# Performance work log

Measured on AMD Instinct MI355X. Metric: run time of the kernel, lower is better.

Reference implementation:

```python
import jax, jax.numpy as jnp
import numpy as np

B, IN_DIM, HID, ATT = 16384, 128, 512, 256
TOTAL = IN_DIM + HID + ATT


def setup_inputs() -> dict:
    key = jax.random.key(0)
    ks = jax.random.split(key, 10)
    u = lambda k, shape, lo, hi: jax.random.uniform(k, shape, jnp.float32, lo, hi)
    return {
        "t": jnp.float32(0.0),
        "h_ltc": jax.random.normal(ks[0], (B, HID), jnp.float32),
        "x_t": jax.random.normal(ks[1], (B, IN_DIM), jnp.float32),
        "context": jax.random.normal(ks[2], (B, ATT), jnp.float32),
        "W_gd": u(ks[3], (2 * HID, TOTAL), -0.1, 0.1),
        "b_gd": u(ks[4], (2 * HID,), -0.1, 0.1),
        "W_tau": u(ks[5], (HID, HID), -0.1, 0.1),
        "b_tau": u(ks[6], (HID,), -0.1, 0.1),
        "gleak": u(ks[7], (HID,), 0.001, 1.0),
        "cm": u(ks[8], (HID,), 0.4, 0.6),
    }


def reference(t, h_ltc, x_t, context, W_gd, b_gd, W_tau, b_tau, gleak, cm):
    # combined: [B, IN+HID+ATT]
    combined = jnp.concatenate([x_t, h_ltc, context], axis=1)
    g_d = combined @ W_gd.T + b_gd            # [B, 2*HID]
    gate, dynamics = jnp.split(g_d, 2, axis=1)
    tau = jax.nn.softplus(h_ltc @ W_tau.T + b_tau)  # [B, HID]
    numerator = jax.nn.sigmoid(gate) * jnp.tanh(dynamics) - h_ltc
    denominator = tau + jax.nn.softplus(cm) + jax.nn.softplus(gleak)
    return numerator / (denominator + 1e-6)
```

## Files before the change

kernel.cpp:

```cpp
#include <hip/hip_runtime.h>
#include <hip/hip_bf16.h>
#include <math.h>

#define BROWS 16384
#define IN_DIM 128
#define HID 512
#define ATT 256
#define KTOT 896
#define KC_TOT 112

typedef __bf16 bf16x8 __attribute__((ext_vector_type(8)));
typedef float f32x4 __attribute__((ext_vector_type(4)));

__global__ void pack_A(const float* __restrict__ x, const float* __restrict__ h,
                       const float* __restrict__ ctx, __hip_bfloat16* __restrict__ A_stage) {
    const int mt = blockIdx.x;
    const int kb = blockIdx.y;
    const float* src; int rs, c0;
    if (kb == 0)      { src = x;   rs = IN_DIM; c0 = 0; }
    else if (kb < 5)  { src = h;   rs = HID;    c0 = (kb - 1) * 128; }
    else              { src = ctx; rs = ATT;    c0 = (kb - 5) * 128; }

    __shared__ __attribute__((aligned(16))) __hip_bfloat16 tile[128][136];

    const int tid = threadIdx.x;
    #pragma unroll
    for (int it = 0; it < 16; ++it) {
        int lin = it * 256 + tid;
        int mi = lin >> 5;
        int c4 = lin & 31;
        float4 v = *(const float4*)(src + (size_t)(mt * 128 + mi) * rs + c0 + c4 * 4);
        union { __hip_bfloat16 hh[4]; ushort4 u; } p;
        p.hh[0] = __float2bfloat16(v.x);
        p.hh[1] = __float2bfloat16(v.y);
        p.hh[2] = __float2bfloat16(v.z);
        p.hh[3] = __float2bfloat16(v.w);
        *(ushort4*)&tile[mi][c4 * 4] = p.u;
    }
    __syncthreads();
    #pragma unroll
    for (int it = 0; it < 8; ++it) {
        int lin = it * 256 + tid;
        int kcl = lin >> 7;
        int mi  = lin & 127;
        uint4 vv = *(const uint4*)&tile[mi][kcl * 8];
        *(uint4*)(A_stage + ((size_t)(mt * KC_TOT + kb * 16 + kcl) * 128 + mi) * 8) = vv;
    }
}

__device__ __forceinline__ float softplus_f(float x) {
    return fmaxf(x, 0.0f) + log1pf(__expf(-fabsf(x)));
}

__global__ void pack_B(const float* __restrict__ W_gd, const float* __restrict__ W_tau,
                       const float* __restrict__ gleak, const float* __restrict__ cm,
                       __hip_bfloat16* __restrict__ B_stage, float* __restrict__ dconst) {
    const int cid = blockIdx.x * 256 + threadIdx.x;
    if (cid < HID) {
        dconst[cid] = softplus_f(cm[cid]) + softplus_f(gleak[cid]) + 1e-6f;
    }
    const int nl = cid % 96;
    const int kc = (cid / 96) % KC_TOT;
    const int jt = cid / (96 * KC_TOT);
    const int jg = nl / 48, type = (nl % 48) / 16, j16 = nl % 16;
    const int j = jt * 32 + jg * 16 + j16;
    const int k0 = kc * 8;

    float v[8];
    if (type == 0) {
        const float* s = W_gd + (size_t)j * KTOT + k0;
        #pragma unroll
        for (int i = 0; i < 8; ++i) v[i] = s[i];
    } else if (type == 1) {
        const float* s = W_gd + (size_t)(HID + j) * KTOT + k0;
        #pragma unroll
        for (int i = 0; i < 8; ++i) v[i] = s[i];
    } else {
        if (k0 >= IN_DIM && k0 < IN_DIM + HID) {
            const float* s = W_tau + (size_t)j * HID + (k0 - IN_DIM);
            #pragma unroll
            for (int i = 0; i < 8; ++i) v[i] = s[i];
        } else {
            #pragma unroll
            for (int i = 0; i < 8; ++i) v[i] = 0.0f;
        }
    }
    union { __hip_bfloat16 hh[8]; uint4 u; } p;
    #pragma unroll
    for (int i = 0; i < 8; ++i) p.hh[i] = __float2bfloat16(v[i]);
    *(uint4*)(B_stage + (size_t)cid * 8) = p.u;
}

__global__ __launch_bounds__(256, 2) void ltc_gemm(
    const __hip_bfloat16* __restrict__ A_stage, const __hip_bfloat16* __restrict__ B_stage,
    const float* __restrict__ h_ltc, const float* __restrict__ b_gd,
    const float* __restrict__ b_tau, const float* __restrict__ dconst,
    float* __restrict__ out) {

    __shared__ __attribute__((aligned(16))) char smem[16384 + 12288];
    char* As = smem;
    char* Bs = smem + 16384;

    const int bx = blockIdx.x;
    const int jt = bx & 15;
    const int mt = bx >> 4;
    const int tid = threadIdx.x;
    const int wave = tid >> 6, lane = tid & 63;
    const int wm = wave >> 1;
    const int wj = wave & 1;
    const int q = lane >> 4, t = lane & 15;

    f32x4 accg[4], accd[4], acct[4];
    #pragma unroll
    for (int i = 0; i < 4; ++i) { accg[i] = (f32x4)0.0f; accd[i] = (f32x4)0.0f; acct[i] = (f32x4)0.0f; }

    const __hip_bfloat16* aSrc[4]; char* aDst[4];
    #pragma unroll
    for (int r = 0; r < 4; ++r) {
        int c = wave + 4 * r;
        int kcl = c >> 1, half = c & 1;
        aSrc[r] = A_stage + ((size_t)(mt * KC_TOT + kcl) * 128 + half * 64 + lane) * 8;
        aDst[r] = As + c * 1024;
    }
    const __hip_bfloat16* bSrc[3]; char* bDst[3];
    #pragma unroll
    for (int r = 0; r < 3; ++r) {
        int c = wave + 4 * r;
        bSrc[r] = B_stage + (size_t)jt * (KC_TOT * 768) + c * 512 + lane * 8;
        bDst[r] = Bs + c * 1024;
    }

    for (int ks = 0; ks < 14; ++ks) {
        #pragma unroll
        for (int r = 0; r < 4; ++r)
            __builtin_amdgcn_global_load_lds(
                (const __attribute__((address_space(1))) void*)aSrc[r],
                (__attribute__((address_space(3))) void*)aDst[r], 16, 0, 0);
        #pragma unroll
        for (int r = 0; r < 3; ++r)
            __builtin_amdgcn_global_load_lds(
                (const __attribute__((address_space(1))) void*)bSrc[r],
                (__attribute__((address_space(3))) void*)bDst[r], 16, 0, 0);
        __syncthreads();

        const bool tau_on = (ks >= 2 && ks < 10);
        #pragma unroll
        for (int ko2 = 0; ko2 < 2; ++ko2) {
            const char* ab = As + (((ko2 * 4 + q) * 128 + wm * 64 + t) << 4);
            bf16x8 a0 = *(const bf16x8*)(ab);
            bf16x8 a1 = *(const bf16x8*)(ab + 256);
            bf16x8 a2 = *(const bf16x8*)(ab + 512);
            bf16x8 a3 = *(const bf16x8*)(ab + 768);
            const char* bb = Bs + (((ko2 * 4 + q) * 96 + wj * 48 + t) << 4);
            bf16x8 bg = *(const bf16x8*)(bb);
            bf16x8 bd = *(const bf16x8*)(bb + 256);
            accg[0] = __builtin_amdgcn_mfma_f32_16x16x32_bf16(a0, bg, accg[0], 0, 0, 0);
            accg[1] = __builtin_amdgcn_mfma_f32_16x16x32_bf16(a1, bg, accg[1], 0, 0, 0);
            accg[2] = __builtin_amdgcn_mfma_f32_16x16x32_bf16(a2, bg, accg[2], 0, 0, 0);
            accg[3] = __builtin_amdgcn_mfma_f32_16x16x32_bf16(a3, bg, accg[3], 0, 0, 0);
            accd[0] = __builtin_amdgcn_mfma_f32_16x16x32_bf16(a0, bd, accd[0], 0, 0, 0);
            accd[1] = __builtin_amdgcn_mfma_f32_16x16x32_bf16(a1, bd, accd[1], 0, 0, 0);
            accd[2] = __builtin_amdgcn_mfma_f32_16x16x32_bf16(a2, bd, accd[2], 0, 0, 0);
            accd[3] = __builtin_amdgcn_mfma_f32_16x16x32_bf16(a3, bd, accd[3], 0, 0, 0);
            if (tau_on) {
                bf16x8 bt = *(const bf16x8*)(bb + 512);
                acct[0] = __builtin_amdgcn_mfma_f32_16x16x32_bf16(a0, bt, acct[0], 0, 0, 0);
                acct[1] = __builtin_amdgcn_mfma_f32_16x16x32_bf16(a1, bt, acct[1], 0, 0, 0);
                acct[2] = __builtin_amdgcn_mfma_f32_16x16x32_bf16(a2, bt, acct[2], 0, 0, 0);
                acct[3] = __builtin_amdgcn_mfma_f32_16x16x32_bf16(a3, bt, acct[3], 0, 0, 0);
            }
        }
        #pragma unroll
        for (int r = 0; r < 4; ++r) aSrc[r] += 8192;
        #pragma unroll
        for (int r = 0; r < 3; ++r) bSrc[r] += 6144;
        __syncthreads();
    }

    const int j = jt * 32 + wj * 16 + t;
    const float bgj = b_gd[j];
    const float bdj = b_gd[HID + j];
    const float btj = b_tau[j];
    const float dcj = dconst[j];
    const int row0 = mt * 128 + wm * 64 + q * 4;
    #pragma unroll
    for (int i = 0; i < 4; ++i) {
        #pragma unroll
        for (int r = 0; r < 4; ++r) {
            const int row = row0 + i * 16 + r;
            const float g  = accg[i][r] + bgj;
            const float d  = accd[i][r] + bdj;
            const float tp = acct[i][r] + btj;
            const float h  = h_ltc[(size_t)row * HID + j];
            const float sig = 1.0f / (1.0f + __expf(-g));
            const float th  = tanhf(d);
            const float tau = fmaxf(tp, 0.0f) + log1pf(__expf(-fabsf(tp)));
            out[(size_t)row * HID + j] = (sig * th - h) / (tau + dcj);
        }
    }
}

extern "C" void kernel_launch(void* const* d_in, const int* in_sizes, int n_in,
                              void* d_out, int out_size, void* d_ws, size_t ws_size,
                              hipStream_t stream) {
    const float* h_ltc = (const float*)d_in[1];
    const float* x_t   = (const float*)d_in[2];
    const float* ctx   = (const float*)d_in[3];
    const float* W_gd  = (const float*)d_in[4];
    const float* b_gd  = (const float*)d_in[5];
    const float* W_tau = (const float*)d_in[6];
    const float* b_tau = (const float*)d_in[7];
    const float* gleak = (const float*)d_in[8];
    const float* cm    = (const float*)d_in[9];

    char* ws = (char*)d_ws;
    __hip_bfloat16* A_stage = (__hip_bfloat16*)ws;
    __hip_bfloat16* B_stage = (__hip_bfloat16*)(ws + 29360128);
    float* dconst = (float*)(ws + 29360128 + 2752512);

    pack_A<<<dim3(128, 7), 256, 0, stream>>>(x_t, h_ltc, ctx, A_stage);
    pack_B<<<672, 256, 0, stream>>>(W_gd, W_tau, gleak, cm, B_stage, dconst);
    ltc_gemm<<<2048, 256, 0, stream>>>(A_stage, B_stage, h_ltc, b_gd, b_tau, dconst,
                                       (float*)d_out);
}
```

Baseline: 190.8 us.

## Double GEMM tile width to 64 columns and use fast epilogue intrinsics

Widens each GEMM block's column tile from 32 to 64 hidden units, so every A tile loaded into LDS feeds twice as many MFMAs, and halves the grid to 1024 blocks. Block order now runs rows first within a column tile. The epilogue swaps tanhf, log1pf and division for exp/rcp/log approximations. The costs are doubled accumulator registers and more LDS per block, which may lower occupancy, plus slightly lower epilogue accuracy.

```diff
diff --git a/kernel.cpp b/kernel.cpp
--- a/kernel.cpp
+++ b/kernel.cpp
@@ -59,11 +59,11 @@
     if (cid < HID) {
         dconst[cid] = softplus_f(cm[cid]) + softplus_f(gleak[cid]) + 1e-6f;
     }
-    const int nl = cid % 96;
-    const int kc = (cid / 96) % KC_TOT;
-    const int jt = cid / (96 * KC_TOT);
+    const int nl = cid % 192;
+    const int kc = (cid / 192) % KC_TOT;
+    const int jt = cid / (192 * KC_TOT);
     const int jg = nl / 48, type = (nl % 48) / 16, j16 = nl % 16;
-    const int j = jt * 32 + jg * 16 + j16;
+    const int j = jt * 64 + jg * 16 + j16;
     const int k0 = kc * 8;
 
     float v[8];
@@ -97,22 +97,26 @@
     const float* __restrict__ b_tau, const float* __restrict__ dconst,
     float* __restrict__ out) {
 
-    __shared__ __attribute__((aligned(16))) char smem[16384 + 12288];
+    __shared__ __attribute__((aligned(16))) char smem[16384 + 24576];
     char* As = smem;
     char* Bs = smem + 16384;
 
     const int bx = blockIdx.x;
-    const int jt = bx & 15;
-    const int mt = bx >> 4;
+    const int mt = bx & 127;
+    const int jt = bx >> 7;
     const int tid = threadIdx.x;
     const int wave = tid >> 6, lane = tid & 63;
     const int wm = wave >> 1;
     const int wj = wave & 1;
     const int q = lane >> 4, t = lane & 15;
 
-    f32x4 accg[4], accd[4], acct[4];
-    #pragma unroll
-    for (int i = 0; i < 4; ++i) { accg[i] = (f32x4)0.0f; accd[i] = (f32x4)0.0f; acct[i] = (f32x4)0.0f; }
+    f32x4 accg[2][4], accd[2][4], acct[2][4];
+    #pragma unroll
+    for (int g = 0; g < 2; ++g)
+        #pragma unroll
+        for (int i = 0; i < 4; ++i) {
+            accg[g][i] = (f32x4)0.0f; accd[g][i] = (f32x4)0.0f; acct[g][i] = (f32x4)0.0f;
+        }
 
     const __hip_bfloat16* aSrc[4]; char* aDst[4];
     #pragma unroll
@@ -122,11 +126,11 @@
         aSrc[r] = A_stage + ((size_t)(mt * KC_TOT + kcl) * 128 + half * 64 + lane) * 8;
         aDst[r] = As + c * 1024;
     }
-    const __hip_bfloat16* bSrc[3]; char* bDst[3];
-    #pragma unroll
-    for (int r = 0; r < 3; ++r) {
+    const __hip_bfloat16* bSrc[6]; char* bDst[6];
+    #pragma unroll
+    for (int r = 0; r < 6; ++r) {
         int c = wave + 4 * r;
-        bSrc[r] = B_stage + (size_t)jt * (KC_TOT * 768) + c * 512 + lane * 8;
+        bSrc[r] = B_stage + (size_t)jt * (KC_TOT * 1536) + c * 512 + lane * 8;
         bDst[r] = Bs + c * 1024;
     }
 
@@ -137,7 +141,7 @@
                 (const __attribute__((address_space(1))) void*)aSrc[r],
                 (__attribute__((address_space(3))) void*)aDst[r], 16, 0, 0);
         #pragma unroll
-        for (int r = 0; r < 3; ++r)
+        for (int r = 0; r < 6; ++r)
             __builtin_amdgcn_global_load_lds(
                 (const __attribute__((address_space(1))) void*)bSrc[r],
                 (__attribute__((address_space(3))) void*)bDst[r], 16, 0, 0);
@@ -146,56 +150,63 @@
         const bool tau_on = (ks >= 2 && ks < 10);
         #pragma unroll
         for (int ko2 = 0; ko2 < 2; ++ko2) {
-            const char* ab = As + (((ko2 * 4 + q) * 128 + wm * 64 + t) << 4);
+            const int kcl = ko2 * 4 + q;
+            const char* ab = As + (((kcl * 128) + wm * 64 + t) << 4);
             bf16x8 a0 = *(const bf16x8*)(ab);
             bf16x8 a1 = *(const bf16x8*)(ab + 256);
             bf16x8 a2 = *(const bf16x8*)(ab + 512);
             bf16x8 a3 = *(const bf16x8*)(ab + 768);
-            const char* bb = Bs + (((ko2 * 4 + q) * 96 + wj * 48 + t) << 4);
-            bf16x8 bg = *(const bf16x8*)(bb);
-            bf16x8 bd = *(const bf16x8*)(bb + 256);
-            accg[0] = __builtin_amdgcn_mfma_f32_16x16x32_bf16(a0, bg, accg[0], 0, 0, 0);
-            accg[1] = __builtin_amdgcn_mfma_f32_16x16x32_bf16(a1, bg, accg[1], 0, 0, 0);
-            accg[2] = __builtin_amdgcn_mfma_f32_16x16x32_bf16(a2, bg, accg[2], 0, 0, 0);
-            accg[3] = __builtin_amdgcn_mfma_f32_16x16x32_bf16(a3, bg, accg[3], 0, 0, 0);
-            accd[0] = __builtin_amdgcn_mfma_f32_16x16x32_bf16(a0, bd, accd[0], 0, 0, 0);
-            accd[1] = __builtin_amdgcn_mfma_f32_16x16x32_bf16(a1, bd, accd[1], 0, 0, 0);
-            accd[2] = __builtin_amdgcn_mfma_f32_16x16x32_bf16(a2, bd, accd[2], 0, 0, 0);
-            accd[3] = __builtin_amdgcn_mfma_f32_16x16x32_bf16(a3, bd, accd[3], 0, 0, 0);
-            if (tau_on) {
-                bf16x8 bt = *(const bf16x8*)(bb + 512);
-                acct[0] = __builtin_amdgcn_mfma_f32_16x16x32_bf16(a0, bt, acct[0], 0, 0, 0);
-                acct[1] = __builtin_amdgcn_mfma_f32_16x16x32_bf16(a1, bt, acct[1], 0, 0, 0);
-                acct[2] = __builtin_amdgcn_mfma_f32_16x16x32_bf16(a2, bt, acct[2], 0, 0, 0);
-                acct[3] = __builtin_amdgcn_mfma_f32_16x16x32_bf16(a3, bt, acct[3], 0, 0, 0);
+            #pragma unroll
+            for (int g = 0; g < 2; ++g) {
+                const char* bb = Bs + (((kcl * 192) + wj * 96 + g * 48 + t) << 4);
+                bf16x8 bg = *(const bf16x8*)(bb);
+                bf16x8 bd = *(const bf16x8*)(bb + 256);
+                accg[g][0] = __builtin_amdgcn_mfma_f32_16x16x32_bf16(a0, bg, accg[g][0], 0, 0, 0);
+                accg[g][1] = __builtin_amdgcn_mfma_f32_16x16x32_bf16(a1, bg, accg[g][1], 0, 0, 0);
+                accg[g][2] = __builtin_amdgcn_mfma_f32_16x16x32_bf16(a2, bg, accg[g][2], 0, 0, 0);
+                accg[g][3] = __builtin_amdgcn_mfma_f32_16x16x32_bf16(a3, bg, accg[g][3], 0, 0, 0);
+                accd[g][0] = __builtin_amdgcn_mfma_f32_16x16x32_bf16(a0, bd, accd[g][0], 0, 0, 0);
+                accd[g][1] = __builtin_amdgcn_mfma_f32_16x16x32_bf16(a1, bd, accd[g][1], 0, 0, 0);
+                accd[g][2] = __builtin_amdgcn_mfma_f32_16x16x32_bf16(a2, bd, accd[g][2], 0, 0, 0);
+                accd[g][3] = __builtin_amdgcn_mfma_f32_16x16x32_bf16(a3, bd, accd[g][3], 0, 0, 0);
+                if (tau_on) {
+                    bf16x8 bt = *(const bf16x8*)(bb + 512);
+                    acct[g][0] = __builtin_amdgcn_mfma_f32_16x16x32_bf16(a0, bt, acct[g][0], 0, 0, 0);
+                    acct[g][1] = __builtin_amdgcn_mfma_f32_16x16x32_bf16(a1, bt, acct[g][1], 0, 0, 0);
+                    acct[g][2] = __builtin_amdgcn_mfma_f32_16x16x32_bf16(a2, bt, acct[g][2], 0, 0, 0);
+                    acct[g][3] = __builtin_amdgcn_mfma_f32_16x16x32_bf16(a3, bt, acct[g][3], 0, 0, 0);
+                }
             }
         }
         #pragma unroll
         for (int r = 0; r < 4; ++r) aSrc[r] += 8192;
         #pragma unroll
-        for (int r = 0; r < 3; ++r) bSrc[r] += 6144;
+        for (int r = 0; r < 6; ++r) bSrc[r] += 12288;
         __syncthreads();
     }
 
-    const int j = jt * 32 + wj * 16 + t;
-    const float bgj = b_gd[j];
-    const float bdj = b_gd[HID + j];
-    const float btj = b_tau[j];
-    const float dcj = dconst[j];
     const int row0 = mt * 128 + wm * 64 + q * 4;
     #pragma unroll
-    for (int i = 0; i < 4; ++i) {
-        #pragma unroll
-        for (int r = 0; r < 4; ++r) {
-            const int row = row0 + i * 16 + r;
-            const float g  = accg[i][r] + bgj;
-            const float d  = accd[i][r] + bdj;
-            const float tp = acct[i][r] + btj;
-            const float h  = h_ltc[(size_t)row * HID + j];
-            const float sig = 1.0f / (1.0f + __expf(-g));
-            const float th  = tanhf(d);
-            const float tau = fmaxf(tp, 0.0f) + log1pf(__expf(-fabsf(tp)));
-            out[(size_t)row * HID + j] = (sig * th - h) / (tau + dcj);
+    for (int g = 0; g < 2; ++g) {
+        const int j = jt * 64 + (wj * 2 + g) * 16 + t;
+        const float bgj = b_gd[j];
+        const float bdj = b_gd[HID + j];
+        const float btj = b_tau[j];
+        const float dcj = dconst[j];
+        #pragma unroll
+        for (int i = 0; i < 4; ++i) {
+            #pragma unroll
+            for (int r = 0; r < 4; ++r) {
+                const int row = row0 + i * 16 + r;
+                const float gv = accg[g][i][r] + bgj;
+                const float dv = accd[g][i][r] + bdj;
+                const float tp = acct[g][i][r] + btj;
+                const float h  = h_ltc[(size_t)row * HID + j];
+                const float sig = __builtin_amdgcn_rcpf(1.0f + __expf(-gv));
+                const float th  = 1.0f - 2.0f * __builtin_amdgcn_rcpf(__expf(2.0f * dv) + 1.0f);
+                const float tau = fmaxf(tp, 0.0f) + __logf(1.0f + __expf(-fabsf(tp)));
+                out[(size_t)row * HID + j] = (sig * th - h) * __builtin_amdgcn_rcpf(tau + dcj);
+            }
         }
     }
 }
@@ -218,8 +229,8 @@
     __hip_bfloat16* B_stage = (__hip_bfloat16*)(ws + 29360128);
     float* dconst = (float*)(ws + 29360128 + 2752512);
 
+    pack_B<<<672, 256, 0, stream>>>(W_gd, W_tau, gleak, cm, B_stage, dconst);
     pack_A<<<dim3(128, 7), 256, 0, stream>>>(x_t, h_ltc, ctx, A_stage);
-    pack_B<<<672, 256, 0, stream>>>(W_gd, W_tau, gleak, cm, B_stage, dconst);
-    ltc_gemm<<<2048, 256, 0, stream>>>(A_stage, B_stage, h_ltc, b_gd, b_tau, dconst,
+    ltc_gemm<<<1024, 256, 0, stream>>>(A_stage, B_stage, h_ltc, b_gd, b_tau, dconst,
                                        (float*)d_out);
 }
```

Measured after the change: 170.7 us. 1.12x faster.
